# Performance work log

Measured on AMD Instinct MI355X. Metric: run time of the kernel, lower is better.

Reference implementation:

```python
import jax, jax.numpy as jnp
import numpy as np

NO, NR, E, D = 50000, 2000, 600000, 128
NEG_SLOPE = 0.2


def setup_inputs() -> dict:
    key = jax.random.key(0)
    ks = jax.random.split(key, 16)
    p = lambda k, shape: jax.random.normal(k, shape, dtype=jnp.float32) * 0.05
    return {
        "x_order": jax.random.normal(ks[0], (NO, D), dtype=jnp.float32),
        "x_rider": jax.random.normal(ks[1], (NR, D), dtype=jnp.float32),
        "order_idx": jax.random.randint(ks[2], (E,), 0, NO),
        "rider_idx": jax.random.randint(ks[3], (E,), 0, NR),
        # GATConv layer 1 (order_input_dim=128 -> hidden_dim=128, heads=1)
        "Ws1": p(ks[4], (D, D)), "Wd1": p(ks[5], (D, D)),
        "as1": p(ks[6], (D,)), "ad1": p(ks[7], (D,)), "b1": jnp.zeros((D,), jnp.float32),
        # GATConv layer 2 (hidden_dim=128 -> output_dim=128, heads=1)
        "Ws2": p(ks[8], (D, D)), "Wd2": p(ks[9], (D, D)),
        "as2": p(ks[10], (D,)), "ad2": p(ks[11], (D,)), "b2": jnp.zeros((D,), jnp.float32),
    }


def _segment_softmax(e, seg, num_segments):
    # numerically-stable softmax over edges grouped by destination node
    m = jax.ops.segment_max(e, seg, num_segments=num_segments)
    ex = jnp.exp(e - m[seg])
    s = jax.ops.segment_sum(ex, seg, num_segments=num_segments)
    return ex / (s[seg] + 1e-16)


def _gat_bipartite(x_src, x_dst, oi, ri, Ws, Wd, a_src, a_dst, b, n_dst):
    # PyG GATConv, heads=1, bipartite (src=order, dst=rider), no self-loops
    hs = x_src @ Ws            # [NO, D]
    hd = x_dst @ Wd            # [NR, D]
    alpha_s = hs @ a_src       # [NO]
    alpha_d = hd @ a_dst       # [NR]
    e = jax.nn.leaky_relu(alpha_s[oi] + alpha_d[ri], NEG_SLOPE)  # [E]
    alpha = _segment_softmax(e, ri, n_dst)                        # [E]
    out = jax.ops.segment_sum(alpha[:, None] * hs[oi], ri, num_segments=n_dst)
    return out + b


def reference(x_order, x_rider, order_idx, rider_idx,
              Ws1, Wd1, as1, ad1, b1, Ws2, Wd2, as2, ad2, b2):
    n_rider = x_rider.shape[0]
    # layer 1: update riders; order features pass through
    r1 = jax.nn.relu(_gat_bipartite(x_order, x_rider, order_idx, rider_idx,
                                    Ws1, Wd1, as1, ad1, b1, n_rider))
    o1 = jax.nn.relu(x_order)
    # layer 2
    r2 = _gat_bipartite(o1, r1, order_idx, rider_idx,
                        Ws2, Wd2, as2, ad2, b2, n_rider)
    # per-edge gather-dot-sigmoid scoring
    scores = jnp.sum(o1[order_idx] * r2[rider_idx], axis=1)
    return jax.nn.sigmoid(scores)
```

## Files before the change

kernel.cpp:

```cpp
#include <hip/hip_runtime.h>
#include <hip/hip_fp16.h>
#include <math.h>

#define NO 50000
#define NR 2000
#define NE 600000
#define D  128
#define NEG_SLOPE 0.2f
#define CAP 512
#define NB 256
#define CH ((NE + NB - 1) / NB)

__global__ void precompute_wv(const float* __restrict__ Ws1, const float* __restrict__ as1,
                              const float* __restrict__ Wd1, const float* __restrict__ ad1,
                              const float* __restrict__ Ws2, const float* __restrict__ as2,
                              const float* __restrict__ Wd2, const float* __restrict__ ad2,
                              float* __restrict__ wsv1, float* __restrict__ wdv1,
                              float* __restrict__ wsv2, float* __restrict__ wdv2) {
    int k = threadIdx.x;
    float s1 = 0.f, d1 = 0.f, s2 = 0.f, d2 = 0.f;
    for (int j = 0; j < D; ++j) {
        s1 += Ws1[k * D + j] * as1[j];
        d1 += Wd1[k * D + j] * ad1[j];
        s2 += Ws2[k * D + j] * as2[j];
        d2 += Wd2[k * D + j] * ad2[j];
    }
    wsv1[k] = s1; wdv1[k] = d1; wsv2[k] = s2; wdv2[k] = d2;
}

__global__ void order_prep(const float* __restrict__ x,
                           const float* __restrict__ wsv1, const float* __restrict__ wsv2,
                           float* __restrict__ as1o, float* __restrict__ as2o,
                           __half* __restrict__ x16, __half* __restrict__ xr16) {
    int wave = (blockIdx.x * blockDim.x + threadIdx.x) >> 6;
    int lane = threadIdx.x & 63;
    if (wave >= NO) return;
    float2 xv = ((const float2*)(x + (size_t)wave * D))[lane];
    float2 w1 = ((const float2*)wsv1)[lane];
    float2 w2 = ((const float2*)wsv2)[lane];
    float rx0 = fmaxf(xv.x, 0.f), rx1 = fmaxf(xv.y, 0.f);
    ((__half2*)(x16  + (size_t)wave * D))[lane] = __floats2half2_rn(xv.x, xv.y);
    ((__half2*)(xr16 + (size_t)wave * D))[lane] = __floats2half2_rn(rx0, rx1);
    float a1 = xv.x * w1.x + xv.y * w1.y;
    float a2 = rx0 * w2.x + rx1 * w2.y;
    for (int off = 32; off; off >>= 1) {
        a1 += __shfl_down(a1, off);
        a2 += __shfl_down(a2, off);
    }
    if (lane == 0) { as1o[wave] = a1; as2o[wave] = a2; }
}

__global__ void rider_alpha(const float* __restrict__ xr, const float* __restrict__ wdv1,
                            float* __restrict__ ad1r) {
    int wave = (blockIdx.x * blockDim.x + threadIdx.x) >> 6;
    int lane = threadIdx.x & 63;
    if (wave >= NR) return;
    const float* row = xr + (size_t)wave * D;
    float a = row[lane] * wdv1[lane] + row[lane + 64] * wdv1[lane + 64];
    for (int off = 32; off; off >>= 1) a += __shfl_down(a, off);
    if (lane == 0) ad1r[wave] = a;
}


__global__ void blockhist_kernel(const int* __restrict__ ri, int* __restrict__ blockHist) {
    __shared__ int h[NR];
    int b = blockIdx.x, t = threadIdx.x;
    for (int i = t; i < NR; i += 256) h[i] = 0;
    __syncthreads();
    int lo = b * CH;
    int hi = lo + CH; if (hi > NE) hi = NE;
    for (int i = lo + t; i < hi; i += 256) atomicAdd(&h[ri[i]], 1);
    __syncthreads();
    for (int i = t; i < NR; i += 256) blockHist[(size_t)b * NR + i] = h[i];
}

__global__ void rowscan_kernel(int* __restrict__ blockHist, int* __restrict__ total) {
    int r = blockIdx.x * blockDim.x + threadIdx.x;
    if (r >= NR) return;
    int run = 0;
    for (int b = 0; b < NB; ++b) {
        int idx = b * NR + r;
        int v = blockHist[idx];
        blockHist[idx] = run;
        run += v;
    }
    total[r] = run;
}

__global__ void scan_kernel(const int* __restrict__ total, int* __restrict__ starts) {
    __shared__ int sums[256];
    int t = threadIdx.x;
    int v[8];
    int s = 0;
    for (int j = 0; j < 8; ++j) {
        int idx = t * 8 + j;
        int c = (idx < NR) ? total[idx] : 0;
        v[j] = s;
        s += c;
    }
    sums[t] = s;
    __syncthreads();
    for (int off = 1; off < 256; off <<= 1) {
        int add = (t >= off) ? sums[t - off] : 0;
        __syncthreads();
        sums[t] += add;
        __syncthreads();
    }
    int base = sums[t] - s;
    for (int j = 0; j < 8; ++j) {
        int idx = t * 8 + j;
        if (idx < NR) starts[idx] = base + v[j];
    }
}

__global__ void scatter_kernel(const int* __restrict__ oi, const int* __restrict__ ri,
                               const int* __restrict__ starts,
                               const int* __restrict__ blockHist,
                               int* __restrict__ sOrd) {
    __shared__ int h[NR];
    int b = blockIdx.x, t = threadIdx.x;
    for (int i = t; i < NR; i += 256) h[i] = 0;
    __syncthreads();
    int lo = b * CH;
    int hi = lo + CH; if (hi > NE) hi = NE;
    for (int i = lo + t; i < hi; i += 256) {
        int r = ri[i];
        int rank = atomicAdd(&h[r], 1);
        int pos = starts[r] + blockHist[(size_t)b * NR + r] + rank;
        sOrd[pos] = oi[i];
    }
}

template <int L>
__global__ void rider_agg(const __half* __restrict__ xg, const float* __restrict__ as_o,
                          const float* __restrict__ ad_r,
                          const int* __restrict__ starts, const int* __restrict__ cnt,
                          const int* __restrict__ sOrd,
                          const float* __restrict__ W, const float* __restrict__ bias,
                          const float* __restrict__ wdv2,
                          float* __restrict__ ad2r, __half* __restrict__ r216) {
    __shared__ float eL[CAP];
    __shared__ int   sO[CAP];
    __shared__ float red[256];
    __shared__ float red8[256][9];
    __shared__ float tl[D];
    int r = blockIdx.x;
    int t = threadIdx.x;
    int base = starts[r], n = cnt[r];
    float ad = ad_r[r];

    float lmax = -1e30f;
    for (int i = t; i < n; i += 256) {
        int o = sOrd[base + i];
        float e = as_o[o] + ad;
        e = (e > 0.f) ? e : NEG_SLOPE * e;
        if (i < CAP) { eL[i] = e; sO[i] = o; }
        lmax = fmaxf(lmax, e);
    }
    red[t] = lmax;
    __syncthreads();
    for (int off = 128; off; off >>= 1) {
        if (t < off) red[t] = fmaxf(red[t], red[t + off]);
        __syncthreads();
    }
    float m = red[0];
    __syncthreads();

    float ls = 0.f;
    for (int i = t; i < n; i += 256) {
        float e;
        if (i < CAP) e = eL[i];
        else {
            int o = sOrd[base + i];
            e = as_o[o] + ad;
            e = (e > 0.f) ? e : NEG_SLOPE * e;
        }
        float ex = __expf(e - m);
        if (i < CAP) eL[i] = ex;
        ls += ex;
    }
    red[t] = ls;
    __syncthreads();
    for (int off = 128; off; off >>= 1) {
        if (t < off) red[t] += red[t + off];
        __syncthreads();
    }
    float inv = 1.f / (red[0] + 1e-16f);
    __syncthreads();

    int grp = t >> 4;
    int lh  = t & 15;
    float acc[8];
#pragma unroll
    for (int k = 0; k < 8; ++k) acc[k] = 0.f;
    for (int i = grp; i < n; i += 16) {
        float a; int o;
        if (i < CAP) { a = eL[i]; o = sO[i]; }
        else {
            o = sOrd[base + i];
            float e = as_o[o] + ad;
            e = (e > 0.f) ? e : NEG_SLOPE * e;
            a = __expf(e - m);
        }
        uint4 hv = ((const uint4*)(xg + (size_t)o * D))[lh];
        float2 f0 = __half22float2(*(const __half2*)&hv.x);
        float2 f1 = __half22float2(*(const __half2*)&hv.y);
        float2 f2 = __half22float2(*(const __half2*)&hv.z);
        float2 f3 = __half22float2(*(const __half2*)&hv.w);
        acc[0] += a * f0.x; acc[1] += a * f0.y;
        acc[2] += a * f1.x; acc[3] += a * f1.y;
        acc[4] += a * f2.x; acc[5] += a * f2.y;
        acc[6] += a * f3.x; acc[7] += a * f3.y;
    }
#pragma unroll
    for (int k = 0; k < 8; ++k) red8[t][k] = acc[k];
    __syncthreads();
    if (t < D) {
        int lh2 = t >> 3, k = t & 7;
        float s = 0.f;
        for (int g = 0; g < 16; ++g) s += red8[g * 16 + lh2][k];
        tl[t] = s * inv;
    }
    __syncthreads();

    int d = t & 127, h = t >> 7;
    float acc2 = 0.f;
    for (int k = h * 64; k < h * 64 + 64; ++k) acc2 += tl[k] * W[k * D + d];
    red[t] = acc2;
    __syncthreads();
    if (L == 1) {
        if (t < 128) red[t] = fmaxf(red[t] + red[t + 128] + bias[t], 0.f) * wdv2[t];
        __syncthreads();
        for (int off = 64; off; off >>= 1) {
            if (t < off) red[t] += red[t + off];
            __syncthreads();
        }
        if (t == 0) ad2r[r] = red[0];
    } else {
        if (t < 128) r216[(size_t)r * D + t] = __float2half(red[t] + red[t + 128] + bias[t]);
    }
}

__global__ void score_edges(const __half* __restrict__ xr16, const __half* __restrict__ r216,
                            const int* __restrict__ oi, const int* __restrict__ ri,
                            float* __restrict__ out) {
    int gid = blockIdx.x * blockDim.x + threadIdx.x;
    int e  = gid >> 4;
    int lh = gid & 15;
    if (e >= NE) return;
    int o = oi[e], r = ri[e];
    uint4 hx = ((const uint4*)(xr16 + (size_t)o * D))[lh];
    uint4 hr = ((const uint4*)(r216 + (size_t)r * D))[lh];
    float2 a0 = __half22float2(*(const __half2*)&hx.x);
    float2 a1 = __half22float2(*(const __half2*)&hx.y);
    float2 a2 = __half22float2(*(const __half2*)&hx.z);
    float2 a3 = __half22float2(*(const __half2*)&hx.w);
    float2 b0 = __half22float2(*(const __half2*)&hr.x);
    float2 b1 = __half22float2(*(const __half2*)&hr.y);
    float2 b2 = __half22float2(*(const __half2*)&hr.z);
    float2 b3 = __half22float2(*(const __half2*)&hr.w);
    float p = a0.x * b0.x + a0.y * b0.y + a1.x * b1.x + a1.y * b1.y +
              a2.x * b2.x + a2.y * b2.y + a3.x * b3.x + a3.y * b3.y;
    p += __shfl_xor(p, 8);
    p += __shfl_xor(p, 4);
    p += __shfl_xor(p, 2);
    p += __shfl_xor(p, 1);
    if (lh == 0) out[e] = 1.f / (1.f + __expf(-p));
}

extern "C" void kernel_launch(void* const* d_in, const int* in_sizes, int n_in,
                              void* d_out, int out_size, void* d_ws, size_t ws_size,
                              hipStream_t stream) {
    const float* x_order = (const float*)d_in[0];
    const float* x_rider = (const float*)d_in[1];
    const int*   oi      = (const int*)d_in[2];
    const int*   ri      = (const int*)d_in[3];
    const float* Ws1 = (const float*)d_in[4];
    const float* Wd1 = (const float*)d_in[5];
    const float* as1 = (const float*)d_in[6];
    const float* ad1 = (const float*)d_in[7];
    const float* b1  = (const float*)d_in[8];
    const float* Ws2 = (const float*)d_in[9];
    const float* Wd2 = (const float*)d_in[10];
    const float* as2 = (const float*)d_in[11];
    const float* ad2 = (const float*)d_in[12];
    const float* b2  = (const float*)d_in[13];
    float* out = (float*)d_out;

    char* w = (char*)d_ws;
    float* wsv1 = (float*)w; w += 512;
    float* wdv1 = (float*)w; w += 512;
    float* wsv2 = (float*)w; w += 512;
    float* wdv2 = (float*)w; w += 512;
    float* as1o = (float*)w; w += (size_t)NO * 4;
    float* as2o = (float*)w; w += (size_t)NO * 4;
    float* ad1r = (float*)w; w += (size_t)NR * 4;
    float* ad2r = (float*)w; w += (size_t)NR * 4;
    int* total  = (int*)w;   w += (size_t)NR * 4;
    int* starts = (int*)w;   w += (size_t)NR * 4;
    int* blockHist = (int*)w; w += (size_t)NB * NR * 4;
    int* sOrd   = (int*)w;   w += (size_t)NE * 4;
    __half* x16  = (__half*)w; w += (size_t)NO * D * 2;
    __half* xr16 = (__half*)w; w += (size_t)NO * D * 2;
    __half* r216 = (__half*)w; w += (size_t)NR * D * 2;

    precompute_wv<<<1, 128, 0, stream>>>(Ws1, as1, Wd1, ad1, Ws2, as2, Wd2, ad2,
                                         wsv1, wdv1, wsv2, wdv2);
    order_prep<<<NO / 4, 256, 0, stream>>>(x_order, wsv1, wsv2, as1o, as2o, x16, xr16);
    rider_alpha<<<NR / 4, 256, 0, stream>>>(x_rider, wdv1, ad1r);

    blockhist_kernel<<<NB, 256, 0, stream>>>(ri, blockHist);
    rowscan_kernel<<<(NR + 255) / 256, 256, 0, stream>>>(blockHist, total);
    scan_kernel<<<1, 256, 0, stream>>>(total, starts);
    scatter_kernel<<<NB, 256, 0, stream>>>(oi, ri, starts, blockHist, sOrd);

    rider_agg<1><<<NR, 256, 0, stream>>>(x16, as1o, ad1r, starts, total, sOrd,
                                         Ws1, b1, wdv2, ad2r, ((__half*)0));
    rider_agg<2><<<NR, 256, 0, stream>>>(xr16, as2o, ad2r, starts, total, sOrd,
                                         Ws2, b2, wdv2, (float*)0, r216);
    score_edges<<<(NE * 16 + 255) / 256, 256, 0, stream>>>(xr16, r216, oi, ri, out);
}
```

Baseline: 242.1 us.

## Fuse layer-2 aggregation with edge scoring and drop relu copy and softmax max

Fuses the second GAT aggregation with per-edge scoring in one per-rider block, caching up to 192 gathered order rows in shared memory for reuse in the score dot products. It also records edge ids during scatter so scores can be written to their original positions. The separate relu'd fp16 copy is removed in favour of applying relu on the fly, the two prep kernels are merged, and the softmax max-subtraction pass is dropped. Dropping the max risks exp overflow for large logits, and the larger shared-memory footprint may lower occupancy.

New measurement: 282.4 us. 16.7% more time.

```diff
diff --git a/kernel.cpp b/kernel.cpp
--- a/kernel.cpp
+++ b/kernel.cpp
@@ -7,7 +7,8 @@
 #define NE 600000
 #define D  128
 #define NEG_SLOPE 0.2f
-#define CAP 512
+#define CAP 448
+#define ROWS 192
 #define NB 256
 #define CH ((NE + NB - 1) / NB)
 
@@ -28,37 +29,34 @@
     wsv1[k] = s1; wdv1[k] = d1; wsv2[k] = s2; wdv2[k] = d2;
 }
 
-__global__ void order_prep(const float* __restrict__ x,
-                           const float* __restrict__ wsv1, const float* __restrict__ wsv2,
-                           float* __restrict__ as1o, float* __restrict__ as2o,
-                           __half* __restrict__ x16, __half* __restrict__ xr16) {
-    int wave = (blockIdx.x * blockDim.x + threadIdx.x) >> 6;
+__global__ void node_prep(const float* __restrict__ x, const float* __restrict__ xr,
+                          const float* __restrict__ wsv1, const float* __restrict__ wsv2,
+                          const float* __restrict__ wdv1,
+                          float* __restrict__ as1o, float* __restrict__ as2o,
+                          float* __restrict__ ad1r, __half* __restrict__ x16) {
     int lane = threadIdx.x & 63;
-    if (wave >= NO) return;
-    float2 xv = ((const float2*)(x + (size_t)wave * D))[lane];
-    float2 w1 = ((const float2*)wsv1)[lane];
-    float2 w2 = ((const float2*)wsv2)[lane];
-    float rx0 = fmaxf(xv.x, 0.f), rx1 = fmaxf(xv.y, 0.f);
-    ((__half2*)(x16  + (size_t)wave * D))[lane] = __floats2half2_rn(xv.x, xv.y);
-    ((__half2*)(xr16 + (size_t)wave * D))[lane] = __floats2half2_rn(rx0, rx1);
-    float a1 = xv.x * w1.x + xv.y * w1.y;
-    float a2 = rx0 * w2.x + rx1 * w2.y;
-    for (int off = 32; off; off >>= 1) {
-        a1 += __shfl_down(a1, off);
-        a2 += __shfl_down(a2, off);
-    }
-    if (lane == 0) { as1o[wave] = a1; as2o[wave] = a2; }
-}
-
-__global__ void rider_alpha(const float* __restrict__ xr, const float* __restrict__ wdv1,
-                            float* __restrict__ ad1r) {
-    int wave = (blockIdx.x * blockDim.x + threadIdx.x) >> 6;
-    int lane = threadIdx.x & 63;
-    if (wave >= NR) return;
-    const float* row = xr + (size_t)wave * D;
-    float a = row[lane] * wdv1[lane] + row[lane + 64] * wdv1[lane + 64];
-    for (int off = 32; off; off >>= 1) a += __shfl_down(a, off);
-    if (lane == 0) ad1r[wave] = a;
+    if (blockIdx.x < NO / 4) {
+        int row = blockIdx.x * 4 + (threadIdx.x >> 6);
+        float2 xv = ((const float2*)(x + (size_t)row * D))[lane];
+        float2 w1 = ((const float2*)wsv1)[lane];
+        float2 w2 = ((const float2*)wsv2)[lane];
+        float rx0 = fmaxf(xv.x, 0.f), rx1 = fmaxf(xv.y, 0.f);
+        ((__half2*)(x16 + (size_t)row * D))[lane] = __floats2half2_rn(xv.x, xv.y);
+        float a1 = xv.x * w1.x + xv.y * w1.y;
+        float a2 = rx0 * w2.x + rx1 * w2.y;
+        for (int off = 32; off; off >>= 1) {
+            a1 += __shfl_down(a1, off);
+            a2 += __shfl_down(a2, off);
+        }
+        if (lane == 0) { as1o[row] = a1; as2o[row] = a2; }
+    } else {
+        int row = (blockIdx.x - NO / 4) * 4 + (threadIdx.x >> 6);
+        float2 xv = ((const float2*)(xr + (size_t)row * D))[lane];
+        float2 w1 = ((const float2*)wdv1)[lane];
+        float a = xv.x * w1.x + xv.y * w1.y;
+        for (int off = 32; off; off >>= 1) a += __shfl_down(a, off);
+        if (lane == 0) ad1r[row] = a;
+    }
 }
 
 
@@ -116,7 +114,7 @@
 __global__ void scatter_kernel(const int* __restrict__ oi, const int* __restrict__ ri,
                                const int* __restrict__ starts,
                                const int* __restrict__ blockHist,
-                               int* __restrict__ sOrd) {
+                               int* __restrict__ sOrd, int* __restrict__ sEid) {
     __shared__ int h[NR];
     int b = blockIdx.x, t = threadIdx.x;
     for (int i = t; i < NR; i += 256) h[i] = 0;
@@ -128,55 +126,32 @@
         int rank = atomicAdd(&h[r], 1);
         int pos = starts[r] + blockHist[(size_t)b * NR + r] + rank;
         sOrd[pos] = oi[i];
-    }
-}
-
-template <int L>
-__global__ void rider_agg(const __half* __restrict__ xg, const float* __restrict__ as_o,
-                          const float* __restrict__ ad_r,
-                          const int* __restrict__ starts, const int* __restrict__ cnt,
-                          const int* __restrict__ sOrd,
-                          const float* __restrict__ W, const float* __restrict__ bias,
-                          const float* __restrict__ wdv2,
-                          float* __restrict__ ad2r, __half* __restrict__ r216) {
+        sEid[pos] = i;
+    }
+}
+
+__global__ void rider_agg1(const __half* __restrict__ x16, const float* __restrict__ as_o,
+                           const float* __restrict__ ad_r,
+                           const int* __restrict__ starts, const int* __restrict__ cnt,
+                           const int* __restrict__ sOrd,
+                           const float* __restrict__ W, const float* __restrict__ bias,
+                           const float* __restrict__ wdv2, float* __restrict__ ad2r) {
     __shared__ float eL[CAP];
     __shared__ int   sO[CAP];
     __shared__ float red[256];
     __shared__ float red8[256][9];
     __shared__ float tl[D];
-    int r = blockIdx.x;
-    int t = threadIdx.x;
+    int r = blockIdx.x, t = threadIdx.x;
     int base = starts[r], n = cnt[r];
     float ad = ad_r[r];
 
-    float lmax = -1e30f;
+    float ls = 0.f;
     for (int i = t; i < n; i += 256) {
         int o = sOrd[base + i];
         float e = as_o[o] + ad;
         e = (e > 0.f) ? e : NEG_SLOPE * e;
-        if (i < CAP) { eL[i] = e; sO[i] = o; }
-        lmax = fmaxf(lmax, e);
-    }
-    red[t] = lmax;
-    __syncthreads();
-    for (int off = 128; off; off >>= 1) {
-        if (t < off) red[t] = fmaxf(red[t], red[t + off]);
-        __syncthreads();
-    }
-    float m = red[0];
-    __syncthreads();
-
-    float ls = 0.f;
-    for (int i = t; i < n; i += 256) {
-        float e;
-        if (i < CAP) e = eL[i];
-        else {
-            int o = sOrd[base + i];
-            e = as_o[o] + ad;
-            e = (e > 0.f) ? e : NEG_SLOPE * e;
-        }
-        float ex = __expf(e - m);
-        if (i < CAP) eL[i] = ex;
+        float ex = __expf(e);
+        if (i < CAP) { eL[i] = ex; sO[i] = o; }
         ls += ex;
     }
     red[t] = ls;
@@ -188,8 +163,7 @@
     float inv = 1.f / (red[0] + 1e-16f);
     __syncthreads();
 
-    int grp = t >> 4;
-    int lh  = t & 15;
+    int grp = t >> 4, lh = t & 15;
     float acc[8];
 #pragma unroll
     for (int k = 0; k < 8; ++k) acc[k] = 0.f;
@@ -200,9 +174,9 @@
             o = sOrd[base + i];
             float e = as_o[o] + ad;
             e = (e > 0.f) ? e : NEG_SLOPE * e;
-            a = __expf(e - m);
-        }
-        uint4 hv = ((const uint4*)(xg + (size_t)o * D))[lh];
+            a = __expf(e);
+        }
+        uint4 hv = ((const uint4*)(x16 + (size_t)o * D))[lh];
         float2 f0 = __half22float2(*(const __half2*)&hv.x);
         float2 f1 = __half22float2(*(const __half2*)&hv.y);
         float2 f2 = __half22float2(*(const __half2*)&hv.z);
@@ -224,48 +198,126 @@
     __syncthreads();
 
     int d = t & 127, h = t >> 7;
-    float acc2 = 0.f;
-    for (int k = h * 64; k < h * 64 + 64; ++k) acc2 += tl[k] * W[k * D + d];
-    red[t] = acc2;
-    __syncthreads();
-    if (L == 1) {
-        if (t < 128) red[t] = fmaxf(red[t] + red[t + 128] + bias[t], 0.f) * wdv2[t];
-        __syncthreads();
-        for (int off = 64; off; off >>= 1) {
-            if (t < off) red[t] += red[t + off];
-            __syncthreads();
-        }
-        if (t == 0) ad2r[r] = red[0];
-    } else {
-        if (t < 128) r216[(size_t)r * D + t] = __float2half(red[t] + red[t + 128] + bias[t]);
-    }
-}
-
-__global__ void score_edges(const __half* __restrict__ xr16, const __half* __restrict__ r216,
-                            const int* __restrict__ oi, const int* __restrict__ ri,
-                            float* __restrict__ out) {
-    int gid = blockIdx.x * blockDim.x + threadIdx.x;
-    int e  = gid >> 4;
-    int lh = gid & 15;
-    if (e >= NE) return;
-    int o = oi[e], r = ri[e];
-    uint4 hx = ((const uint4*)(xr16 + (size_t)o * D))[lh];
-    uint4 hr = ((const uint4*)(r216 + (size_t)r * D))[lh];
-    float2 a0 = __half22float2(*(const __half2*)&hx.x);
-    float2 a1 = __half22float2(*(const __half2*)&hx.y);
-    float2 a2 = __half22float2(*(const __half2*)&hx.z);
-    float2 a3 = __half22float2(*(const __half2*)&hx.w);
-    float2 b0 = __half22float2(*(const __half2*)&hr.x);
-    float2 b1 = __half22float2(*(const __half2*)&hr.y);
-    float2 b2 = __half22float2(*(const __half2*)&hr.z);
-    float2 b3 = __half22float2(*(const __half2*)&hr.w);
-    float p = a0.x * b0.x + a0.y * b0.y + a1.x * b1.x + a1.y * b1.y +
-              a2.x * b2.x + a2.y * b2.y + a3.x * b3.x + a3.y * b3.y;
-    p += __shfl_xor(p, 8);
-    p += __shfl_xor(p, 4);
-    p += __shfl_xor(p, 2);
-    p += __shfl_xor(p, 1);
-    if (lh == 0) out[e] = 1.f / (1.f + __expf(-p));
+    float a2 = 0.f;
+    for (int k = h * 64; k < h * 64 + 64; ++k) a2 += tl[k] * W[k * D + d];
+    red[t] = a2;
+    __syncthreads();
+    if (t < 128) red[t] = fmaxf(red[t] + red[t + 128] + bias[t], 0.f) * wdv2[t];
+    __syncthreads();
+    for (int off = 64; off; off >>= 1) {
+        if (t < off) red[t] += red[t + off];
+        __syncthreads();
+    }
+    if (t == 0) ad2r[r] = red[0];
+}
+
+__global__ void agg2_score(const __half* __restrict__ x16, const float* __restrict__ as_o,
+                           const float* __restrict__ ad_r,
+                           const int* __restrict__ starts, const int* __restrict__ cnt,
+                           const int* __restrict__ sOrd, const int* __restrict__ sEid,
+                           const float* __restrict__ W, const float* __restrict__ bias,
+                           float* __restrict__ out) {
+    __shared__ __half rowsL[ROWS * D];
+    __shared__ float eL[CAP];
+    __shared__ int   sO[CAP];
+    __shared__ int   sE[CAP];
+    __shared__ float red[256];
+    __shared__ float red8[256][9];
+    __shared__ float tl[D];
+    __shared__ float r2L[D];
+    int r = blockIdx.x, t = threadIdx.x;
+    int base = starts[r], n = cnt[r];
+    float ad = ad_r[r];
+
+    float ls = 0.f;
+    for (int i = t; i < n; i += 256) {
+        int o = sOrd[base + i];
+        float e = as_o[o] + ad;
+        e = (e > 0.f) ? e : NEG_SLOPE * e;
+        float ex = __expf(e);
+        if (i < CAP) { eL[i] = ex; sO[i] = o; sE[i] = sEid[base + i]; }
+        ls += ex;
+    }
+    red[t] = ls;
+    __syncthreads();
+    for (int off = 128; off; off >>= 1) {
+        if (t < off) red[t] += red[t + off];
+        __syncthreads();
+    }
+    float inv = 1.f / (red[0] + 1e-16f);
+    __syncthreads();
+
+    int grp = t >> 4, lh = t & 15;
+    float acc[8];
+#pragma unroll
+    for (int k = 0; k < 8; ++k) acc[k] = 0.f;
+    for (int i = grp; i < n; i += 16) {
+        float a; int o;
+        if (i < CAP) { a = eL[i]; o = sO[i]; }
+        else {
+            o = sOrd[base + i];
+            float e = as_o[o] + ad;
+            e = (e > 0.f) ? e : NEG_SLOPE * e;
+            a = __expf(e);
+        }
+        uint4 hv = ((const uint4*)(x16 + (size_t)o * D))[lh];
+        if (i < ROWS) ((uint4*)rowsL)[i * 16 + lh] = hv;
+        float2 f0 = __half22float2(*(const __half2*)&hv.x);
+        float2 f1 = __half22float2(*(const __half2*)&hv.y);
+        float2 f2 = __half22float2(*(const __half2*)&hv.z);
+        float2 f3 = __half22float2(*(const __half2*)&hv.w);
+        acc[0] += a * fmaxf(f0.x, 0.f); acc[1] += a * fmaxf(f0.y, 0.f);
+        acc[2] += a * fmaxf(f1.x, 0.f); acc[3] += a * fmaxf(f1.y, 0.f);
+        acc[4] += a * fmaxf(f2.x, 0.f); acc[5] += a * fmaxf(f2.y, 0.f);
+        acc[6] += a * fmaxf(f3.x, 0.f); acc[7] += a * fmaxf(f3.y, 0.f);
+    }
+#pragma unroll
+    for (int k = 0; k < 8; ++k) red8[t][k] = acc[k];
+    __syncthreads();
+    if (t < D) {
+        int lh2 = t >> 3, k = t & 7;
+        float s = 0.f;
+        for (int g = 0; g < 16; ++g) s += red8[g * 16 + lh2][k];
+        tl[t] = s * inv;
+    }
+    __syncthreads();
+
+    int d = t & 127, h = t >> 7;
+    float a2 = 0.f;
+    for (int k = h * 64; k < h * 64 + 64; ++k) a2 += tl[k] * W[k * D + d];
+    red[t] = a2;
+    __syncthreads();
+    if (t < 128) r2L[t] = red[t] + red[t + 128] + bias[t];
+    __syncthreads();
+
+    float rv[8];
+#pragma unroll
+    for (int k = 0; k < 8; ++k) rv[k] = r2L[lh * 8 + k];
+
+    for (int i = grp; i < n; i += 16) {
+        uint4 hv;
+        if (i < ROWS) hv = ((const uint4*)rowsL)[i * 16 + lh];
+        else {
+            int o = (i < CAP) ? sO[i] : sOrd[base + i];
+            hv = ((const uint4*)(x16 + (size_t)o * D))[lh];
+        }
+        float2 f0 = __half22float2(*(const __half2*)&hv.x);
+        float2 f1 = __half22float2(*(const __half2*)&hv.y);
+        float2 f2 = __half22float2(*(const __half2*)&hv.z);
+        float2 f3 = __half22float2(*(const __half2*)&hv.w);
+        float p = fmaxf(f0.x, 0.f) * rv[0] + fmaxf(f0.y, 0.f) * rv[1] +
+                  fmaxf(f1.x, 0.f) * rv[2] + fmaxf(f1.y, 0.f) * rv[3] +
+                  fmaxf(f2.x, 0.f) * rv[4] + fmaxf(f2.y, 0.f) * rv[5] +
+                  fmaxf(f3.x, 0.f) * rv[6] + fmaxf(f3.y, 0.f) * rv[7];
+        p += __shfl_xor(p, 8);
+        p += __shfl_xor(p, 4);
+        p += __shfl_xor(p, 2);
+        p += __shfl_xor(p, 1);
+        if (lh == 0) {
+            int eid = (i < CAP) ? sE[i] : sEid[base + i];
+            out[eid] = 1.f / (1.f + __expf(-p));
+        }
+    }
 }
 
 extern "C" void kernel_launch(void* const* d_in, const int* in_sizes, int n_in,
@@ -300,23 +352,21 @@
     int* starts = (int*)w;   w += (size_t)NR * 4;
     int* blockHist = (int*)w; w += (size_t)NB * NR * 4;
     int* sOrd   = (int*)w;   w += (size_t)NE * 4;
+    int* sEid   = (int*)w;   w += (size_t)NE * 4;
     __half* x16  = (__half*)w; w += (size_t)NO * D * 2;
-    __half* xr16 = (__half*)w; w += (size_t)NO * D * 2;
-    __half* r216 = (__half*)w; w += (size_t)NR * D * 2;
 
     precompute_wv<<<1, 128, 0, stream>>>(Ws1, as1, Wd1, ad1, Ws2, as2, Wd2, ad2,
                                          wsv1, wdv1, wsv2, wdv2);
-    order_prep<<<NO / 4, 256, 0, stream>>>(x_order, wsv1, wsv2, as1o, as2o, x16, xr16);
-    rider_alpha<<<NR / 4, 256, 0, stream>>>(x_rider, wdv1, ad1r);
+    node_prep<<<NO / 4 + NR / 4, 256, 0, stream>>>(x_order, x_rider, wsv1, wsv2, wdv1,
+                                                   as1o, as2o, ad1r, x16);
 
     blockhist_kernel<<<NB, 256, 0, stream>>>(ri, blockHist);
     rowscan_kernel<<<(NR + 255) / 256, 256, 0, stream>>>(blockHist, total);
     scan_kernel<<<1, 256, 0, stream>>>(total, starts);
-    scatter_kernel<<<NB, 256, 0, stream>>>(oi, ri, starts, blockHist, sOrd);
-
-    rider_agg<1><<<NR, 256, 0, stream>>>(x16, as1o, ad1r, starts, total, sOrd,
-                                         Ws1, b1, wdv2, ad2r, ((__half*)0));
-    rider_agg<2><<<NR, 256, 0, stream>>>(xr16, as2o, ad2r, starts, total, sOrd,
-                                         Ws2, b2, wdv2, (float*)0, r216);
-    score_edges<<<(NE * 16 + 255) / 256, 256, 0, stream>>>(xr16, r216, oi, ri, out);
-}
+    scatter_kernel<<<NB, 256, 0, stream>>>(oi, ri, starts, blockHist, sOrd, sEid);
+
+    rider_agg1<<<NR, 256, 0, stream>>>(x16, as1o, ad1r, starts, total, sOrd,
+                                       Ws1, b1, wdv2, ad2r);
+    agg2_score<<<NR, 256, 0, stream>>>(x16, as2o, ad2r, starts, total, sOrd, sEid,
+                                       Ws2, b2, out);
+}
```
